# Optimization experiments

Hardware: AMD Instinct MI355X
Metric: run time of the kernel (lower is better)

The kernel has to match this reference:

```python
import jax, jax.numpy as jnp
import numpy as np

NUM_LAYERS = 4
HID = 512
BATCH = 32
SEQ = 2048


def log_g(x):
    # log of the g() activation used by minGRU: g(x) = x+0.5 for x>=0, sigmoid(x) for x<0
    return jnp.where(x >= 0, jnp.log(jax.nn.relu(x) + 0.5), -jax.nn.softplus(-x))


def parallel_scan_log(log_coeffs, log_values):
    # log_coeffs: (B, T, H), log_values: (B, T+1, H); returns h: (B, T, H)
    a_star = jnp.cumsum(jnp.pad(log_coeffs, ((0, 0), (1, 0), (0, 0))), axis=1)  # (B, T+1, H)
    log_h = a_star + jax.lax.cumlogsumexp(log_values - a_star, axis=1)
    return jnp.exp(log_h)[:, 1:]


def setup_inputs() -> dict:
    key = jax.random.key(0)
    ks = jax.random.split(key, 4)
    x = jax.random.normal(ks[0], (BATCH, SEQ, HID), dtype=jnp.float32)
    h0 = jax.random.uniform(ks[1], (NUM_LAYERS, BATCH, HID), dtype=jnp.float32)
    scale = 0.02
    Wz = jax.random.normal(ks[2], (NUM_LAYERS, HID, HID), dtype=jnp.float32) * scale
    Wh = jax.random.normal(ks[3], (NUM_LAYERS, HID, HID), dtype=jnp.float32) * scale
    bz = jnp.zeros((NUM_LAYERS, HID), dtype=jnp.float32)
    bh = jnp.zeros((NUM_LAYERS, HID), dtype=jnp.float32)
    gamma = jnp.ones((NUM_LAYERS, HID), dtype=jnp.float32)
    beta = jnp.zeros((NUM_LAYERS, HID), dtype=jnp.float32)
    return {"x": x, "h0": h0, "Wz": Wz, "bz": bz, "Wh": Wh, "bh": bh, "gamma": gamma, "beta": beta}


def layernorm(x, g, b, eps=1e-5):
    mu = jnp.mean(x, axis=-1, keepdims=True)
    var = jnp.mean((x - mu) ** 2, axis=-1, keepdims=True)
    return (x - mu) * jax.lax.rsqrt(var + eps) * g + b


def reference(x, h0, Wz, bz, Wh, bh, gamma, beta):
    cur = x
    hiddens = []
    L = Wz.shape[0]
    for i in range(L):
        k = jnp.einsum('btd,dh->bth', cur, Wz[i]) + bz[i]
        log_z = -jax.nn.softplus(-k)          # log(sigmoid(k)) = log(z)
        log_coeffs = -jax.nn.softplus(k)      # log(1-z)
        log_tilde_h = log_g(jnp.einsum('btd,dh->bth', cur, Wh[i]) + bh[i])
        log_h0 = log_g(h0[i])[:, None, :]     # (B, 1, H)
        log_values = jnp.concatenate([log_h0, log_z + log_tilde_h], axis=1)
        h = parallel_scan_log(log_coeffs, log_values)  # (B, T, H)
        hiddens.append(h[:, -1])
        out = layernorm(h, gamma[i], beta[i])
        cur = out + cur  # res_proj is Identity since input_size == hidden_size
    return cur, jnp.stack(hiddens, axis=0)
```

## Files before the change

### kernel.cpp

```cpp
#include <hip/hip_runtime.h>
#include <stdint.h>

typedef unsigned short u16;
typedef __bf16 bf16x8 __attribute__((ext_vector_type(8)));
typedef float f32x4 __attribute__((ext_vector_type(4)));

#define HID 512
#define BATCH 32
#define SEQ 2048
#define NLAYERS 4
#define BT (BATCH*SEQ)
#define CHUNKS 64
#define TC (SEQ/CHUNKS)

__device__ __forceinline__ float bf2f(uint32_t lo) {
  union { uint32_t u; float f; } c; c.u = lo << 16; return c.f;
}
__device__ __forceinline__ uint32_t f2bf(float f) {
  union { float f; uint32_t u; } c; c.f = f;
  return (c.u + 0x7fffu + ((c.u >> 16) & 1u)) >> 16;
}
__device__ __forceinline__ float fast_rcp(float x) { return __builtin_amdgcn_rcpf(x); }

__device__ __forceinline__ void gload_lds16(const u16* g, u16* l) {
  __builtin_amdgcn_global_load_lds((__attribute__((address_space(1))) void*)g,
                                   (__attribute__((address_space(3))) void*)l, 16, 0, 0);
}

__global__ __launch_bounds__(256) void conv_weights(const float* __restrict__ Wz,
                                                    const float* __restrict__ Wh,
                                                    u16* __restrict__ Wt) {
  __shared__ float tile[64][65];
  const int l = blockIdx.z;
  const int k0 = blockIdx.x * 64;
  const int n0 = blockIdx.y * 64;
  const float* W = (n0 < 512 ? Wz : Wh) + (size_t)l * HID * HID;
  const int nc0 = (n0 < 512) ? n0 : n0 - 512;
  const int tx = threadIdx.x & 63, ty = threadIdx.x >> 6;
  for (int r = ty; r < 64; r += 4) tile[r][tx] = W[(size_t)(k0 + r) * HID + nc0 + tx];
  __syncthreads();
  for (int r = ty; r < 64; r += 4)
    Wt[((size_t)l * 1024 + n0 + r) * HID + k0 + tx] = (u16)f2bf(tile[tx][r]);
}

__global__ __launch_bounds__(256) void conv_x(const float* __restrict__ x, u16* __restrict__ xb) {
  size_t i = ((size_t)blockIdx.x * 256 + threadIdx.x) * 4;
  float4 f = *(const float4*)(x + i);
  uint2 o;
  o.x = f2bf(f.x) | (f2bf(f.y) << 16);
  o.y = f2bf(f.z) | (f2bf(f.w) << 16);
  *(uint2*)(xb + i) = o;
}

__global__ __launch_bounds__(512) void gemm_av(const u16* __restrict__ Ab,
                                               const u16* __restrict__ Btw,
                                               const float* __restrict__ bz,
                                               const float* __restrict__ bhp,
                                               uint32_t* __restrict__ av,
                                               float* __restrict__ Ac,
                                               float* __restrict__ Bc) {
  __shared__ __align__(16) u16 As[2][2][8192];
  __shared__ __align__(16) u16 Bs[2][2][8192];

  const int bid = blockIdx.x;
  const int xcd = bid & 7, rr_ = bid >> 3;
  const int mt = (rr_ >> 2) * 8 + xcd;
  const int nt = rr_ & 3;
  const int m0 = mt * 256;

  const int tid = threadIdx.x;
  const int lane = tid & 63, wv = tid >> 6;
  const int wm = wv >> 2, wn = wv & 3;
  const int l15 = lane & 15, quad = lane >> 4;
  const int rx = l15 & 7;
  const int bhalf = wn >> 1;

  const int aro0 = l15 * 64 + ((quad ^ rx) * 8);
  const int aro1 = l15 * 64 + (((4 + quad) ^ rx) * 8);
  const int bro0 = ((wn & 1) * 64 + l15) * 64 + ((quad ^ rx) * 8);
  const int bro1 = ((wn & 1) * 64 + l15) * 64 + (((4 + quad) ^ rx) * 8);

  const int srow = tid >> 3;
  const int kslot = (lane & 7) ^ (srow & 7);
  const u16* aS = Ab + (size_t)(m0 + srow) * HID + kslot * 8;
  const int qb = (srow >> 5) & 1, jb = srow & 31;
  const u16* bS = Btw + (size_t)(qb * 512 + nt * 128 + jb) * HID + kslot * 8;

  f32x4 acc[8][4];
#pragma unroll
  for (int i = 0; i < 8; ++i)
#pragma unroll
    for (int j = 0; j < 4; ++j) acc[i][j] = (f32x4){0.f, 0.f, 0.f, 0.f};
  bf16x8 afr[4][2], bfr[4][2];

#define STG_A(T, H, D) if ((T) < 8) { \
    gload_lds16(aS + (size_t)((H)*65536 + (T)*64), &As[D][H][wv*512]); \
    gload_lds16(aS + (size_t)((H)*65536 + 32768 + (T)*64), &As[D][H][4096 + wv*512]); }
#define STG_B(T, H, D) if ((T) < 8) { \
    gload_lds16(bS + (size_t)((H)*32768 + (T)*64), &Bs[D][H][wv*512]); \
    gload_lds16(bS + (size_t)((H)*32768 + 16384 + (T)*64), &Bs[D][H][4096 + wv*512]); }
#define LDA4(D, MB) { \
    _Pragma("unroll") for (int m_ = 0; m_ < 4; ++m_) \
    _Pragma("unroll") for (int k_ = 0; k_ < 2; ++k_) \
      afr[m_][k_] = *(const bf16x8*)&As[D][wm][((MB)+m_)*1024 + (k_ ? aro1 : aro0)]; }
#define LDB2(D, NB) { \
    _Pragma("unroll") for (int n_ = 0; n_ < 2; ++n_) \
    _Pragma("unroll") for (int k_ = 0; k_ < 2; ++k_) \
      bfr[(NB)+n_][k_] = *(const bf16x8*)&Bs[D][bhalf][((NB)+n_)*1024 + (k_ ? bro1 : bro0)]; }
#define QUAD(MB, NB) { \
    _Pragma("unroll") for (int k_ = 0; k_ < 2; ++k_) \
    _Pragma("unroll") for (int m_ = 0; m_ < 4; ++m_) \
    _Pragma("unroll") for (int n_ = 0; n_ < 2; ++n_) \
      acc[(MB)+m_][(NB)+n_] = __builtin_amdgcn_mfma_f32_16x16x32_bf16( \
          afr[m_][k_], bfr[(NB)+n_][k_], acc[(MB)+m_][(NB)+n_], 0, 0, 0); }
#define PH_MID \
    __builtin_amdgcn_s_barrier(); \
    asm volatile("s_waitcnt lgkmcnt(0)" ::: "memory"); \
    __builtin_amdgcn_sched_barrier(0); \
    __builtin_amdgcn_s_setprio(1);
#define PH_END \
    __builtin_amdgcn_s_setprio(0); \
    __builtin_amdgcn_s_barrier(); \
    __builtin_amdgcn_sched_barrier(0);
#define PH_END_VM(N) \
    __builtin_amdgcn_s_setprio(0); \
    asm volatile("s_waitcnt vmcnt(" #N ")" ::: "memory"); \
    __builtin_amdgcn_s_barrier(); \
    __builtin_amdgcn_sched_barrier(0);

  STG_A(0, 0, 0); STG_A(0, 1, 0);
  STG_B(0, 0, 0); STG_B(0, 1, 0);
  STG_B(1, 0, 1); STG_B(1, 1, 1);
  asm volatile("s_waitcnt vmcnt(4)" ::: "memory");
  __builtin_amdgcn_s_barrier();
  __builtin_amdgcn_sched_barrier(0);

#pragma unroll
  for (int it = 0; it < 4; ++it) {
    const int ta = 2 * it, tb = 2 * it + 1;
    LDA4(0, 0); LDB2(0, 0); STG_A(tb, 0, 1);
    PH_MID; QUAD(0, 0); PH_END;
    LDB2(0, 2); STG_A(tb, 1, 1);
    PH_MID; QUAD(0, 2); PH_END;
    LDA4(0, 4); STG_B(ta + 2, 0, 0);
    PH_MID; QUAD(4, 0); PH_END;
    STG_B(ta + 2, 1, 0);
    PH_MID; QUAD(4, 2);
    if (it == 3) { PH_END_VM(0); } else { PH_END_VM(4); }
    LDA4(1, 0); LDB2(1, 0); STG_A(ta + 2, 0, 0);
    PH_MID; QUAD(0, 0); PH_END;
    LDB2(1, 2); STG_A(ta + 2, 1, 0);
    PH_MID; QUAD(0, 2); PH_END;
    LDA4(1, 4); STG_B(tb + 2, 0, 1);
    PH_MID; QUAD(4, 0); PH_END;
    STG_B(tb + 2, 1, 1);
    PH_MID; QUAD(4, 2); PH_END_VM(4);
  }

  const int colbase = nt * 128 + wn * 32;
  float bzv[2], bhv[2];
#pragma unroll
  for (int nf = 0; nf < 2; ++nf) {
    bzv[nf] = bz[colbase + nf * 16 + l15];
    bhv[nf] = bhp[colbase + nf * 16 + l15];
  }
  const int wrow0 = m0 + wm * 128;
  const int bb = wrow0 >> 11;
#pragma unroll
  for (int c = 0; c < 4; ++c) {
    const int cc = ((wrow0 + c * 32) & 2047) >> 5;
    const size_t abase = (size_t)(bb * CHUNKS + cc) * HID;
#pragma unroll
    for (int nf = 0; nf < 2; ++nf) {
      const int col = colbase + nf * 16 + l15;
      float Aseg[2], Bseg[2];
#pragma unroll
      for (int hseg = 0; hseg < 2; ++hseg) {
        const int mf = 2 * c + hseg;
        const int rbase = wrow0 + mf * 16 + quad * 4;
        float A = 1.f, Bv = 0.f;
#pragma unroll
        for (int r = 0; r < 4; ++r) {
          float kv = acc[mf][nf][r] + bzv[nf];
          float hv = acc[mf][nf + 2][r] + bhv[nf];
          float e = __expf(-kv);
          float inv = fast_rcp(1.f + e);
          float a = e * inv;
          float v = inv * ((hv >= 0.f) ? (hv + 0.5f) : fast_rcp(1.f + __expf(-hv)));
          av[(size_t)(rbase + r) * HID + col] = f2bf(a) | (f2bf(v) << 16);
          A *= a;
          Bv = a * Bv + v;
        }
        Aseg[hseg] = A; Bseg[hseg] = Bv;
      }
#pragma unroll
      for (int hseg = 0; hseg < 2; ++hseg) {
        float Ap = __shfl_xor(Aseg[hseg], 16), Bp = __shfl_xor(Bseg[hseg], 16);
        float Ae = (quad & 1) ? Ap : Aseg[hseg], Be = (quad & 1) ? Bp : Bseg[hseg];
        float Al = (quad & 1) ? Aseg[hseg] : Ap, Bl = (quad & 1) ? Bseg[hseg] : Bp;
        Aseg[hseg] = Al * Ae; Bseg[hseg] = Al * Be + Bl;
        Ap = __shfl_xor(Aseg[hseg], 32); Bp = __shfl_xor(Bseg[hseg], 32);
        Ae = (quad & 2) ? Ap : Aseg[hseg]; Be = (quad & 2) ? Bp : Bseg[hseg];
        Al = (quad & 2) ? Aseg[hseg] : Ap; Bl = (quad & 2) ? Bseg[hseg] : Bp;
        Aseg[hseg] = Al * Ae; Bseg[hseg] = Al * Be + Bl;
      }
      float CA = Aseg[1] * Aseg[0];
      float CB = Aseg[1] * Bseg[0] + Bseg[1];
      if (quad == 0) {
        Ac[abase + col] = CA;
        Bc[abase + col] = CB;
      }
    }
  }
#undef STG_A
#undef STG_B
#undef LDA4
#undef LDB2
#undef QUAD
#undef PH_MID
#undef PH_END
#undef PH_END_VM
}

__global__ __launch_bounds__(256) void scan_boundary(const float* __restrict__ Ac,
                                                     const float* __restrict__ Bc,
                                                     const float* __restrict__ h0,
                                                     float* __restrict__ hinit,
                                                     float* __restrict__ hid_out) {
  const int idx = blockIdx.x * 256 + threadIdx.x;
  const int b = idx >> 9, h = idx & 511;
  float x0 = h0[idx];
  float hr = (x0 >= 0.f) ? (x0 + 0.5f) : fast_rcp(1.f + __expf(-x0));
  for (int c = 0; c < CHUNKS; ++c) {
    size_t o = ((size_t)(b * CHUNKS + c)) * HID + h;
    hinit[o] = hr;
    hr = Ac[o] * hr + Bc[o];
  }
  hid_out[idx] = hr;
}

__global__ __launch_bounds__(512) void scan_apply(const uint32_t* av,
                                                  const float* __restrict__ hinit,
                                                  const u16* __restrict__ resb,
                                                  const float* __restrict__ gamma,
                                                  const float* __restrict__ beta,
                                                  u16* outb, float* outf) {
  __shared__ float hbuf[TC][HID];
  const int b = blockIdx.y, c = blockIdx.x, h = threadIdx.x;
  const int lane = h & 63, wv = h >> 6;
  const size_t rowbase = (size_t)(b * SEQ + c * TC) * HID;

  float hr = hinit[((size_t)(b * CHUNKS + c)) * HID + h];
#pragma unroll 8
  for (int t = 0; t < TC; ++t) {
    uint32_t p = av[rowbase + (size_t)t * HID + h];
    hr = bf2f(p & 0xffffu) * hr + bf2f(p >> 16);
    hbuf[t][h] = hr;
  }
  __syncthreads();

  const int h0c = lane * 8;
  const f32x4 gm0 = *(const f32x4*)&gamma[h0c];
  const f32x4 gm1 = *(const f32x4*)&gamma[h0c + 4];
  const f32x4 be0 = *(const f32x4*)&beta[h0c];
  const f32x4 be1 = *(const f32x4*)&beta[h0c + 4];
#pragma unroll
  for (int i = 0; i < 4; ++i) {
    const int t = wv * 4 + i;
    f32x4 v0 = *(const f32x4*)&hbuf[t][h0c];
    f32x4 v1 = *(const f32x4*)&hbuf[t][h0c + 4];
    float s = v0[0] + v0[1] + v0[2] + v0[3] + v1[0] + v1[1] + v1[2] + v1[3];
    float q = v0[0]*v0[0] + v0[1]*v0[1] + v0[2]*v0[2] + v0[3]*v0[3]
            + v1[0]*v1[0] + v1[1]*v1[1] + v1[2]*v1[2] + v1[3]*v1[3];
#pragma unroll
    for (int d = 32; d; d >>= 1) { s += __shfl_xor(s, d); q += __shfl_xor(q, d); }
    const float mu = s * (1.f / HID);
    const float rs = rsqrtf(q * (1.f / HID) - mu * mu + 1e-5f);
    const size_t o = rowbase + (size_t)t * HID + h0c;
    uint4 rr = *(const uint4*)(resb + o);
    float y[8];
    const uint32_t rw[4] = {rr.x, rr.y, rr.z, rr.w};
#pragma unroll
    for (int j = 0; j < 8; ++j) {
      float hv = (j < 4) ? v0[j] : v1[j - 4];
      float gmv = (j < 4) ? gm0[j] : gm1[j - 4];
      float bev = (j < 4) ? be0[j] : be1[j - 4];
      float rv = bf2f((rw[j >> 1] >> ((j & 1) * 16)) & 0xffffu);
      y[j] = (hv - mu) * rs * gmv + bev + rv;
    }
    if (outb) {
      uint4 ob;
      ob.x = f2bf(y[0]) | (f2bf(y[1]) << 16);
      ob.y = f2bf(y[2]) | (f2bf(y[3]) << 16);
      ob.z = f2bf(y[4]) | (f2bf(y[5]) << 16);
      ob.w = f2bf(y[6]) | (f2bf(y[7]) << 16);
      *(uint4*)(outb + o) = ob;
    }
    if (outf) {
      f32x4 o0 = {y[0], y[1], y[2], y[3]}, o1 = {y[4], y[5], y[6], y[7]};
      *(f32x4*)(outf + o) = o0;
      *(f32x4*)(outf + o + 4) = o1;
    }
  }
}

extern "C" void kernel_launch(void* const* d_in, const int* in_sizes, int n_in,
                              void* d_out, int out_size, void* d_ws, size_t ws_size,
                              hipStream_t stream) {
  (void)in_sizes; (void)n_in; (void)out_size; (void)ws_size;
  const float* x     = (const float*)d_in[0];
  const float* h0    = (const float*)d_in[1];
  const float* Wz    = (const float*)d_in[2];
  const float* bz    = (const float*)d_in[3];
  const float* Wh    = (const float*)d_in[4];
  const float* bh    = (const float*)d_in[5];
  const float* gamma = (const float*)d_in[6];
  const float* beta  = (const float*)d_in[7];

  float* outf = (float*)d_out;
  uint32_t* av = (uint32_t*)d_out;

  char* ws = (char*)d_ws;
  u16* curb = (u16*)ws;                                   size_t off = (size_t)BT * HID * 2;
  u16* Wt = (u16*)(ws + off);                             off += (size_t)NLAYERS * 1024 * HID * 2;
  float* Ac = (float*)(ws + off);                         off += (size_t)BATCH * CHUNKS * HID * 4;
  float* Bc = (float*)(ws + off);                         off += (size_t)BATCH * CHUNKS * HID * 4;
  float* hinit = (float*)(ws + off);

  hipLaunchKernelGGL(conv_weights, dim3(8, 16, NLAYERS), dim3(256), 0, stream, Wz, Wh, Wt);
  hipLaunchKernelGGL(conv_x, dim3(BT * HID / 1024), dim3(256), 0, stream, x, curb);

  for (int l = 0; l < NLAYERS; ++l) {
    const bool last = (l == NLAYERS - 1);
    hipLaunchKernelGGL(gemm_av, dim3(1024), dim3(512), 0, stream,
                       curb, Wt + (size_t)l * 1024 * HID, bz + l * HID, bh + l * HID,
                       av, Ac, Bc);
    hipLaunchKernelGGL(scan_boundary, dim3(BATCH * HID / 256), dim3(256), 0, stream,
                       Ac, Bc, h0 + (size_t)l * BATCH * HID, hinit,
                       outf + (size_t)BT * HID + (size_t)l * BATCH * HID);
    hipLaunchKernelGGL(scan_apply, dim3(CHUNKS, BATCH), dim3(512), 0, stream,
                       av, hinit, curb, gamma + l * HID, beta + l * HID,
                       last ? nullptr : curb, last ? outf : nullptr);
  }
}
```

Before: 825.4 us.

## Make GEMM persistent over four M tiles with prefetch overlapping epilogue; use packed bf16 convert

The GEMM kernel now launches 256 blocks, and each block loops over four M tiles. It issues the first K-step loads for the next tile before running the current tile's activation/scan epilogue, so global loads overlap epilogue math and the pipeline fill cost is paid less often. Manual round-to-nearest bf16 packing is replaced with the hardware v_cvt_pk_bf16_f32 instruction in three places. The trade-off is fewer blocks (256 on a 256-CU part, one wave-set per CU), so idle tails and lower latency hiding are possible, and the new instruction's rounding could differ slightly.

```diff
diff --git a/kernel.cpp b/kernel.cpp
--- a/kernel.cpp
+++ b/kernel.cpp
@@ -19,6 +19,11 @@
 __device__ __forceinline__ uint32_t f2bf(float f) {
   union { float f; uint32_t u; } c; c.f = f;
   return (c.u + 0x7fffu + ((c.u >> 16) & 1u)) >> 16;
+}
+__device__ __forceinline__ uint32_t pk_bf16(float lo, float hi) {
+  uint32_t r;
+  asm("v_cvt_pk_bf16_f32 %0, %1, %2" : "=v"(r) : "v"(lo), "v"(hi));
+  return r;
 }
 __device__ __forceinline__ float fast_rcp(float x) { return __builtin_amdgcn_rcpf(x); }
 
@@ -47,8 +52,8 @@
   size_t i = ((size_t)blockIdx.x * 256 + threadIdx.x) * 4;
   float4 f = *(const float4*)(x + i);
   uint2 o;
-  o.x = f2bf(f.x) | (f2bf(f.y) << 16);
-  o.y = f2bf(f.z) | (f2bf(f.w) << 16);
+  o.x = pk_bf16(f.x, f.y);
+  o.y = pk_bf16(f.z, f.w);
   *(uint2*)(xb + i) = o;
 }
 
@@ -63,10 +68,8 @@
   __shared__ __align__(16) u16 Bs[2][2][8192];
 
   const int bid = blockIdx.x;
-  const int xcd = bid & 7, rr_ = bid >> 3;
-  const int mt = (rr_ >> 2) * 8 + xcd;
-  const int nt = rr_ & 3;
-  const int m0 = mt * 256;
+  const int xcd = bid & 7, s = bid >> 3;
+  const int nt = s & 3, mg = s >> 2;
 
   const int tid = threadIdx.x;
   const int lane = tid & 63, wv = tid >> 6;
@@ -82,20 +85,15 @@
 
   const int srow = tid >> 3;
   const int kslot = (lane & 7) ^ (srow & 7);
-  const u16* aS = Ab + (size_t)(m0 + srow) * HID + kslot * 8;
   const int qb = (srow >> 5) & 1, jb = srow & 31;
   const u16* bS = Btw + (size_t)(qb * 512 + nt * 128 + jb) * HID + kslot * 8;
 
   f32x4 acc[8][4];
-#pragma unroll
-  for (int i = 0; i < 8; ++i)
-#pragma unroll
-    for (int j = 0; j < 4; ++j) acc[i][j] = (f32x4){0.f, 0.f, 0.f, 0.f};
   bf16x8 afr[4][2], bfr[4][2];
 
-#define STG_A(T, H, D) if ((T) < 8) { \
-    gload_lds16(aS + (size_t)((H)*65536 + (T)*64), &As[D][H][wv*512]); \
-    gload_lds16(aS + (size_t)((H)*65536 + 32768 + (T)*64), &As[D][H][4096 + wv*512]); }
+#define STG_A(P, T, H, D) if ((T) < 8) { \
+    gload_lds16((P) + (size_t)((H)*65536 + (T)*64), &As[D][H][wv*512]); \
+    gload_lds16((P) + (size_t)((H)*65536 + 32768 + (T)*64), &As[D][H][4096 + wv*512]); }
 #define STG_B(T, H, D) if ((T) < 8) { \
     gload_lds16(bS + (size_t)((H)*32768 + (T)*64), &Bs[D][H][wv*512]); \
     gload_lds16(bS + (size_t)((H)*32768 + 16384 + (T)*64), &Bs[D][H][4096 + wv*512]); }
@@ -128,88 +126,117 @@
     __builtin_amdgcn_s_barrier(); \
     __builtin_amdgcn_sched_barrier(0);
 
-  STG_A(0, 0, 0); STG_A(0, 1, 0);
-  STG_B(0, 0, 0); STG_B(0, 1, 0);
-  STG_B(1, 0, 1); STG_B(1, 1, 1);
-  asm volatile("s_waitcnt vmcnt(4)" ::: "memory");
-  __builtin_amdgcn_s_barrier();
-  __builtin_amdgcn_sched_barrier(0);
-
-#pragma unroll
-  for (int it = 0; it < 4; ++it) {
-    const int ta = 2 * it, tb = 2 * it + 1;
-    LDA4(0, 0); LDB2(0, 0); STG_A(tb, 0, 1);
-    PH_MID; QUAD(0, 0); PH_END;
-    LDB2(0, 2); STG_A(tb, 1, 1);
-    PH_MID; QUAD(0, 2); PH_END;
-    LDA4(0, 4); STG_B(ta + 2, 0, 0);
-    PH_MID; QUAD(4, 0); PH_END;
-    STG_B(ta + 2, 1, 0);
-    PH_MID; QUAD(4, 2);
-    if (it == 3) { PH_END_VM(0); } else { PH_END_VM(4); }
-    LDA4(1, 0); LDB2(1, 0); STG_A(ta + 2, 0, 0);
-    PH_MID; QUAD(0, 0); PH_END;
-    LDB2(1, 2); STG_A(ta + 2, 1, 0);
-    PH_MID; QUAD(0, 2); PH_END;
-    LDA4(1, 4); STG_B(tb + 2, 0, 1);
-    PH_MID; QUAD(4, 0); PH_END;
-    STG_B(tb + 2, 1, 1);
-    PH_MID; QUAD(4, 2); PH_END_VM(4);
-  }
-
-  const int colbase = nt * 128 + wn * 32;
-  float bzv[2], bhv[2];
-#pragma unroll
-  for (int nf = 0; nf < 2; ++nf) {
-    bzv[nf] = bz[colbase + nf * 16 + l15];
-    bhv[nf] = bhp[colbase + nf * 16 + l15];
-  }
-  const int wrow0 = m0 + wm * 128;
-  const int bb = wrow0 >> 11;
-#pragma unroll
-  for (int c = 0; c < 4; ++c) {
-    const int cc = ((wrow0 + c * 32) & 2047) >> 5;
-    const size_t abase = (size_t)(bb * CHUNKS + cc) * HID;
+  {
+    const int mt0 = (mg * 4) * 8 + xcd;
+    const u16* aS0 = Ab + (size_t)(mt0 * 256 + srow) * HID + kslot * 8;
+    STG_A(aS0, 0, 0, 0); STG_A(aS0, 0, 1, 0);
+    STG_B(0, 0, 0); STG_B(0, 1, 0);
+    STG_B(1, 0, 1); STG_B(1, 1, 1);
+    asm volatile("s_waitcnt vmcnt(4)" ::: "memory");
+    __builtin_amdgcn_s_barrier();
+    __builtin_amdgcn_sched_barrier(0);
+  }
+
+  for (int rep = 0; rep < 4; ++rep) {
+    const int mt = (mg * 4 + rep) * 8 + xcd;
+    const int m0 = mt * 256;
+    const u16* aS = Ab + (size_t)(m0 + srow) * HID + kslot * 8;
+
+#pragma unroll
+    for (int i = 0; i < 8; ++i)
+#pragma unroll
+      for (int j = 0; j < 4; ++j) acc[i][j] = (f32x4){0.f, 0.f, 0.f, 0.f};
+
+#pragma unroll
+    for (int it = 0; it < 4; ++it) {
+      const int ta = 2 * it, tb = 2 * it + 1;
+      LDA4(0, 0); LDB2(0, 0); STG_A(aS, tb, 0, 1);
+      PH_MID; QUAD(0, 0); PH_END;
+      LDB2(0, 2); STG_A(aS, tb, 1, 1);
+      PH_MID; QUAD(0, 2); PH_END;
+      LDA4(0, 4); STG_B(ta + 2, 0, 0);
+      PH_MID; QUAD(4, 0); PH_END;
+      STG_B(ta + 2, 1, 0);
+      PH_MID; QUAD(4, 2);
+      if (it == 3) { PH_END_VM(0); } else { PH_END_VM(4); }
+      LDA4(1, 0); LDB2(1, 0); STG_A(aS, ta + 2, 0, 0);
+      PH_MID; QUAD(0, 0); PH_END;
+      LDB2(1, 2); STG_A(aS, ta + 2, 1, 0);
+      PH_MID; QUAD(0, 2); PH_END;
+      LDA4(1, 4); STG_B(tb + 2, 0, 1);
+      PH_MID; QUAD(4, 0); PH_END;
+      STG_B(tb + 2, 1, 1);
+      PH_MID; QUAD(4, 2); PH_END_VM(4);
+    }
+
+    if (rep < 3) {
+      const int mtn = (mg * 4 + rep + 1) * 8 + xcd;
+      const u16* aSn = Ab + (size_t)(mtn * 256 + srow) * HID + kslot * 8;
+      STG_A(aSn, 0, 0, 0); STG_A(aSn, 0, 1, 0);
+      STG_B(0, 0, 0); STG_B(0, 1, 0);
+      STG_B(1, 0, 1); STG_B(1, 1, 1);
+    }
+
+    const int colbase = nt * 128 + wn * 32;
+    float bzv[2], bhv[2];
 #pragma unroll
     for (int nf = 0; nf < 2; ++nf) {
-      const int col = colbase + nf * 16 + l15;
-      float Aseg[2], Bseg[2];
-#pragma unroll
-      for (int hseg = 0; hseg < 2; ++hseg) {
-        const int mf = 2 * c + hseg;
-        const int rbase = wrow0 + mf * 16 + quad * 4;
-        float A = 1.f, Bv = 0.f;
-#pragma unroll
-        for (int r = 0; r < 4; ++r) {
-          float kv = acc[mf][nf][r] + bzv[nf];
-          float hv = acc[mf][nf + 2][r] + bhv[nf];
-          float e = __expf(-kv);
-          float inv = fast_rcp(1.f + e);
-          float a = e * inv;
-          float v = inv * ((hv >= 0.f) ? (hv + 0.5f) : fast_rcp(1.f + __expf(-hv)));
-          av[(size_t)(rbase + r) * HID + col] = f2bf(a) | (f2bf(v) << 16);
-          A *= a;
-          Bv = a * Bv + v;
+      bzv[nf] = bz[colbase + nf * 16 + l15];
+      bhv[nf] = bhp[colbase + nf * 16 + l15];
+    }
+    const int wrow0 = m0 + wm * 128;
+    const int bb = wrow0 >> 11;
+#pragma unroll
+    for (int c = 0; c < 4; ++c) {
+      const int cc = ((wrow0 + c * 32) & 2047) >> 5;
+      const size_t abase = (size_t)(bb * CHUNKS + cc) * HID;
+#pragma unroll
+      for (int nf = 0; nf < 2; ++nf) {
+        const int col = colbase + nf * 16 + l15;
+        float Aseg[2], Bseg[2];
+#pragma unroll
+        for (int hseg = 0; hseg < 2; ++hseg) {
+          const int mf = 2 * c + hseg;
+          const int rbase = wrow0 + mf * 16 + quad * 4;
+          float A = 1.f, Bv = 0.f;
+#pragma unroll
+          for (int r = 0; r < 4; ++r) {
+            float kv = acc[mf][nf][r] + bzv[nf];
+            float hv = acc[mf][nf + 2][r] + bhv[nf];
+            float e = __expf(-kv);
+            float inv = fast_rcp(1.f + e);
+            float a = e * inv;
+            float v = inv * ((hv >= 0.f) ? (hv + 0.5f) : fast_rcp(1.f + __expf(-hv)));
+            av[(size_t)(rbase + r) * HID + col] = pk_bf16(a, v);
+            A *= a;
+            Bv = a * Bv + v;
+          }
+          Aseg[hseg] = A; Bseg[hseg] = Bv;
         }
-        Aseg[hseg] = A; Bseg[hseg] = Bv;
+#pragma unroll
+        for (int hseg = 0; hseg < 2; ++hseg) {
+          float Ap = __shfl_xor(Aseg[hseg], 16), Bp = __shfl_xor(Bseg[hseg], 16);
+          float Ae = (quad & 1) ? Ap : Aseg[hseg], Be = (quad & 1) ? Bp : Bseg[hseg];
+          float Al = (quad & 1) ? Aseg[hseg] : Ap, Bl = (quad & 1) ? Bseg[hseg] : Bp;
+          Aseg[hseg] = Al * Ae; Bseg[hseg] = Al * Be + Bl;
+          Ap = __shfl_xor(Aseg[hseg], 32); Bp = __shfl_xor(Bseg[hseg], 32);
+          Ae = (quad & 2) ? Ap : Aseg[hseg]; Be = (quad & 2) ? Bp : Bseg[hseg];
+          Al = (quad & 2) ? Aseg[hseg] : Ap; Bl = (quad & 2) ? Bseg[hseg] : Bp;
+          Aseg[hseg] = Al * Ae; Bseg[hseg] = Al * Be + Bl;
+        }
+        float CA = Aseg[1] * Aseg[0];
+        float CB = Aseg[1] * Bseg[0] + Bseg[1];
+        if (quad == 0) {
+          Ac[abase + col] = CA;
+          Bc[abase + col] = CB;
+        }
       }
-#pragma unroll
-      for (int hseg = 0; hseg < 2; ++hseg) {
-        float Ap = __shfl_xor(Aseg[hseg], 16), Bp = __shfl_xor(Bseg[hseg], 16);
-        float Ae = (quad & 1) ? Ap : Aseg[hseg], Be = (quad & 1) ? Bp : Bseg[hseg];
-        float Al = (quad & 1) ? Aseg[hseg] : Ap, Bl = (quad & 1) ? Bseg[hseg] : Bp;
-        Aseg[hseg] = Al * Ae; Bseg[hseg] = Al * Be + Bl;
-        Ap = __shfl_xor(Aseg[hseg], 32); Bp = __shfl_xor(Bseg[hseg], 32);
-        Ae = (quad & 2) ? Ap : Aseg[hseg]; Be = (quad & 2) ? Bp : Bseg[hseg];
-        Al = (quad & 2) ? Aseg[hseg] : Ap; Bl = (quad & 2) ? Bseg[hseg] : Bp;
-        Aseg[hseg] = Al * Ae; Bseg[hseg] = Al * Be + Bl;
-      }
-      float CA = Aseg[1] * Aseg[0];
-      float CB = Aseg[1] * Bseg[0] + Bseg[1];
-      if (quad == 0) {
-        Ac[abase + col] = CA;
-        Bc[abase + col] = CB;
-      }
+    }
+
+    if (rep < 3) {
+      asm volatile("s_waitcnt vmcnt(0) lgkmcnt(0)" ::: "memory");
+      __builtin_amdgcn_s_barrier();
+      __builtin_amdgcn_sched_barrier(0);
     }
   }
 #undef STG_A
@@ -290,10 +317,10 @@
     }
     if (outb) {
       uint4 ob;
-      ob.x = f2bf(y[0]) | (f2bf(y[1]) << 16);
-      ob.y = f2bf(y[2]) | (f2bf(y[3]) << 16);
-      ob.z = f2bf(y[4]) | (f2bf(y[5]) << 16);
-      ob.w = f2bf(y[6]) | (f2bf(y[7]) << 16);
+      ob.x = pk_bf16(y[0], y[1]);
+      ob.y = pk_bf16(y[2], y[3]);
+      ob.z = pk_bf16(y[4], y[5]);
+      ob.w = pk_bf16(y[6], y[7]);
       *(uint4*)(outb + o) = ob;
     }
     if (outf) {
@@ -332,7 +359,7 @@
 
   for (int l = 0; l < NLAYERS; ++l) {
     const bool last = (l == NLAYERS - 1);
-    hipLaunchKernelGGL(gemm_av, dim3(1024), dim3(512), 0, stream,
+    hipLaunchKernelGGL(gemm_av, dim3(256), dim3(512), 0, stream,
                        curb, Wt + (size_t)l * 1024 * HID, bz + l * HID, bh + l * HID,
                        av, Ac, Bc);
     hipLaunchKernelGGL(scan_boundary, dim3(BATCH * HID / 256), dim3(256), 0, stream,
```

New measurement: 1.035 ms. +25.3%, slower.

## Store chunk-local prefix coefficients in GEMM epilogue to remove sequential scan in apply

Applied to the files above, without the earlier changes.

The GEMM epilogue now computes an intra-chunk prefix of the (a, v) affine recurrence using shuffle-up scans across quads and segments. It stores the cumulative (A, B) per row as packed bf16, so that h = A*hinit + B can be evaluated independently per timestep. scan_apply then drops its serial 32-step loop and the LDS buffer and barrier, evaluating h directly with vectorised loads. Hardware packed bf16 conversion replaces the manual rounding. The risk is lower precision, because cumulative products are now quantised to bf16, and a slightly heavier epilogue.

```diff
diff --git a/kernel.cpp b/kernel.cpp
--- a/kernel.cpp
+++ b/kernel.cpp
@@ -19,6 +19,11 @@
 __device__ __forceinline__ uint32_t f2bf(float f) {
   union { float f; uint32_t u; } c; c.f = f;
   return (c.u + 0x7fffu + ((c.u >> 16) & 1u)) >> 16;
+}
+__device__ __forceinline__ uint32_t pk_bf16(float lo, float hi) {
+  uint32_t r;
+  asm("v_cvt_pk_bf16_f32 %0, %1, %2" : "=v"(r) : "v"(lo), "v"(hi));
+  return r;
 }
 __device__ __forceinline__ float fast_rcp(float x) { return __builtin_amdgcn_rcpf(x); }
 
@@ -47,8 +52,8 @@
   size_t i = ((size_t)blockIdx.x * 256 + threadIdx.x) * 4;
   float4 f = *(const float4*)(x + i);
   uint2 o;
-  o.x = f2bf(f.x) | (f2bf(f.y) << 16);
-  o.y = f2bf(f.z) | (f2bf(f.w) << 16);
+  o.x = pk_bf16(f.x, f.y);
+  o.y = pk_bf16(f.z, f.w);
   *(uint2*)(xb + i) = o;
 }
 
@@ -173,11 +178,10 @@
 #pragma unroll
     for (int nf = 0; nf < 2; ++nf) {
       const int col = colbase + nf * 16 + l15;
-      float Aseg[2], Bseg[2];
+      float aar[2][4], vvr[2][4], SA[2], SB[2];
 #pragma unroll
       for (int hseg = 0; hseg < 2; ++hseg) {
         const int mf = 2 * c + hseg;
-        const int rbase = wrow0 + mf * 16 + quad * 4;
         float A = 1.f, Bv = 0.f;
 #pragma unroll
         for (int r = 0; r < 4; ++r) {
@@ -187,28 +191,45 @@
           float inv = fast_rcp(1.f + e);
           float a = e * inv;
           float v = inv * ((hv >= 0.f) ? (hv + 0.5f) : fast_rcp(1.f + __expf(-hv)));
-          av[(size_t)(rbase + r) * HID + col] = f2bf(a) | (f2bf(v) << 16);
+          aar[hseg][r] = a; vvr[hseg][r] = v;
           A *= a;
           Bv = a * Bv + v;
         }
-        Aseg[hseg] = A; Bseg[hseg] = Bv;
+        SA[hseg] = A; SB[hseg] = Bv;
       }
 #pragma unroll
       for (int hseg = 0; hseg < 2; ++hseg) {
-        float Ap = __shfl_xor(Aseg[hseg], 16), Bp = __shfl_xor(Bseg[hseg], 16);
-        float Ae = (quad & 1) ? Ap : Aseg[hseg], Be = (quad & 1) ? Bp : Bseg[hseg];
-        float Al = (quad & 1) ? Aseg[hseg] : Ap, Bl = (quad & 1) ? Bseg[hseg] : Bp;
-        Aseg[hseg] = Al * Ae; Bseg[hseg] = Al * Be + Bl;
-        Ap = __shfl_xor(Aseg[hseg], 32); Bp = __shfl_xor(Bseg[hseg], 32);
-        Ae = (quad & 2) ? Ap : Aseg[hseg]; Be = (quad & 2) ? Bp : Bseg[hseg];
-        Al = (quad & 2) ? Aseg[hseg] : Ap; Bl = (quad & 2) ? Bseg[hseg] : Bp;
-        Aseg[hseg] = Al * Ae; Bseg[hseg] = Al * Be + Bl;
+        float iA = SA[hseg], iB = SB[hseg];
+        float pA = __shfl_up(iA, 16), pB = __shfl_up(iB, 16);
+        if (quad >= 1) { iB = iA * pB + iB; iA = iA * pA; }
+        pA = __shfl_up(iA, 32); pB = __shfl_up(iB, 32);
+        if (quad >= 2) { iB = iA * pB + iB; iA = iA * pA; }
+        SA[hseg] = iA; SB[hseg] = iB;
       }
-      float CA = Aseg[1] * Aseg[0];
-      float CB = Aseg[1] * Bseg[0] + Bseg[1];
-      if (quad == 0) {
-        Ac[abase + col] = CA;
-        Bc[abase + col] = CB;
+      float E0A = __shfl_up(SA[0], 16), E0B = __shfl_up(SB[0], 16);
+      if (quad == 0) { E0A = 1.f; E0B = 0.f; }
+      float T0A = __shfl(SA[0], 48 + l15), T0B = __shfl(SB[0], 48 + l15);
+      float e1A = __shfl_up(SA[1], 16), e1B = __shfl_up(SB[1], 16);
+      if (quad == 0) { e1A = 1.f; e1B = 0.f; }
+      float E1A = e1A * T0A, E1B = e1A * T0B + e1B;
+#pragma unroll
+      for (int hseg = 0; hseg < 2; ++hseg) {
+        const float EA = hseg ? E1A : E0A;
+        const float EB = hseg ? E1B : E0B;
+        const int rbase = wrow0 + (2 * c + hseg) * 16 + quad * 4;
+        float Ar = 1.f, Br = 0.f;
+#pragma unroll
+        for (int r = 0; r < 4; ++r) {
+          Ar = aar[hseg][r] * Ar;
+          Br = aar[hseg][r] * Br + vvr[hseg][r];
+          float PA = Ar * EA;
+          float PB = Ar * EB + Br;
+          av[(size_t)(rbase + r) * HID + col] = pk_bf16(PA, PB);
+          if (hseg == 1 && r == 3 && quad == 3) {
+            Ac[abase + col] = PA;
+            Bc[abase + col] = PB;
+          }
+        }
       }
     }
   }
@@ -245,55 +266,55 @@
                                                   const float* __restrict__ gamma,
                                                   const float* __restrict__ beta,
                                                   u16* outb, float* outf) {
-  __shared__ float hbuf[TC][HID];
-  const int b = blockIdx.y, c = blockIdx.x, h = threadIdx.x;
-  const int lane = h & 63, wv = h >> 6;
+  const int b = blockIdx.y, c = blockIdx.x;
+  const int lane = threadIdx.x & 63, wv = threadIdx.x >> 6;
   const size_t rowbase = (size_t)(b * SEQ + c * TC) * HID;
-
-  float hr = hinit[((size_t)(b * CHUNKS + c)) * HID + h];
-#pragma unroll 8
-  for (int t = 0; t < TC; ++t) {
-    uint32_t p = av[rowbase + (size_t)t * HID + h];
-    hr = bf2f(p & 0xffffu) * hr + bf2f(p >> 16);
-    hbuf[t][h] = hr;
-  }
-  __syncthreads();
-
   const int h0c = lane * 8;
+
+  const size_t hib = ((size_t)(b * CHUNKS + c)) * HID + h0c;
+  const f32x4 hi0 = *(const f32x4*)&hinit[hib];
+  const f32x4 hi1 = *(const f32x4*)&hinit[hib + 4];
   const f32x4 gm0 = *(const f32x4*)&gamma[h0c];
   const f32x4 gm1 = *(const f32x4*)&gamma[h0c + 4];
   const f32x4 be0 = *(const f32x4*)&beta[h0c];
   const f32x4 be1 = *(const f32x4*)&beta[h0c + 4];
+
 #pragma unroll
   for (int i = 0; i < 4; ++i) {
     const int t = wv * 4 + i;
-    f32x4 v0 = *(const f32x4*)&hbuf[t][h0c];
-    f32x4 v1 = *(const f32x4*)&hbuf[t][h0c + 4];
-    float s = v0[0] + v0[1] + v0[2] + v0[3] + v1[0] + v1[1] + v1[2] + v1[3];
-    float q = v0[0]*v0[0] + v0[1]*v0[1] + v0[2]*v0[2] + v0[3]*v0[3]
-            + v1[0]*v1[0] + v1[1]*v1[1] + v1[2]*v1[2] + v1[3]*v1[3];
+    const size_t o = rowbase + (size_t)t * HID + h0c;
+    const uint4 p0 = *(const uint4*)(av + o);
+    const uint4 p1 = *(const uint4*)(av + o + 4);
+    const uint32_t pw[8] = {p0.x, p0.y, p0.z, p0.w, p1.x, p1.y, p1.z, p1.w};
+    float hv[8];
+#pragma unroll
+    for (int j = 0; j < 8; ++j) {
+      const float hij = (j < 4) ? hi0[j] : hi1[j - 4];
+      hv[j] = bf2f(pw[j] & 0xffffu) * hij + bf2f(pw[j] >> 16);
+    }
+    float s = hv[0] + hv[1] + hv[2] + hv[3] + hv[4] + hv[5] + hv[6] + hv[7];
+    float q = hv[0]*hv[0] + hv[1]*hv[1] + hv[2]*hv[2] + hv[3]*hv[3]
+            + hv[4]*hv[4] + hv[5]*hv[5] + hv[6]*hv[6] + hv[7]*hv[7];
 #pragma unroll
     for (int d = 32; d; d >>= 1) { s += __shfl_xor(s, d); q += __shfl_xor(q, d); }
     const float mu = s * (1.f / HID);
     const float rs = rsqrtf(q * (1.f / HID) - mu * mu + 1e-5f);
-    const size_t o = rowbase + (size_t)t * HID + h0c;
-    uint4 rr = *(const uint4*)(resb + o);
+    const uint4 rr = *(const uint4*)(resb + o);
+    const uint32_t rw[4] = {rr.x, rr.y, rr.z, rr.w};
     float y[8];
-    const uint32_t rw[4] = {rr.x, rr.y, rr.z, rr.w};
 #pragma unroll
     for (int j = 0; j < 8; ++j) {
-      float hv = (j < 4) ? v0[j] : v1[j - 4];
-      float gmv = (j < 4) ? gm0[j] : gm1[j - 4];
-      float bev = (j < 4) ? be0[j] : be1[j - 4];
-      float rv = bf2f((rw[j >> 1] >> ((j & 1) * 16)) & 0xffffu);
-      y[j] = (hv - mu) * rs * gmv + bev + rv;
+      const float gmv = (j < 4) ? gm0[j] : gm1[j - 4];
+      const float bev = (j < 4) ? be0[j] : be1[j - 4];
+      const float rv = bf2f((rw[j >> 1] >> ((j & 1) * 16)) & 0xffffu);
+      y[j] = (hv[j] - mu) * rs * gmv + bev + rv;
     }
     if (outb) {
       uint4 ob;
-      ob.x = f2bf(y[0]) | (f2bf(y[1]) << 16);
-      ob.y = f2bf(y[2]) | (f2bf(y[3]) << 16);
-      ob.z = f2bf(y[4]) | (f2bf(y[5]) << 16);
-      ob.w = f2bf(y[6]) | (f2bf(y[7]) << 16);
+      ob.x = pk_bf16(y[0], y[1]);
+      ob.y = pk_bf16(y[2], y[3]);
+      ob.z = pk_bf16(y[4], y[5]);
+      ob.w = pk_bf16(y[6], y[7]);
       *(uint4*)(outb + o) = ob;
     }
     if (outf) {
```

New measurement: 835.5 us. No clear change (+1.2%).
